# Performance work log

Hardware: AMD Instinct MI355X
Metric: run time of the kernel (lower is better)

## Reference

```python
import jax, jax.numpy as jnp
import numpy as np

P_BU = 0.5  # y_bottom_up_percent
P_TD = 1.0 - P_BU
EPS = 1e-12


def l2n(w):
    # F.normalize(w, dim=1)
    n = jnp.linalg.norm(w, axis=1, keepdims=True)
    return w / jnp.maximum(n, EPS)


def setup_inputs() -> dict:
    key = jax.random.key(0)
    ks = jax.random.split(key, 5)
    X, Y, Z = 64 * 64, 16384, 100
    return {
        "x": jax.random.normal(ks[0], (1, 64, 64), dtype=jnp.float32),
        "z": jax.random.randint(ks[1], (1,), 0, Z, dtype=jnp.int64 if jax.config.jax_enable_x64 else jnp.int32).astype(jnp.int32),
        "per_item": 10,
        "x2y_w": jax.random.uniform(ks[2], (Y, X), dtype=jnp.float32),
        "z2y_w": jax.random.uniform(ks[3], (Y, Z), dtype=jnp.float32),
        "y2z_w": jax.random.uniform(ks[4], (Z, Y), dtype=jnp.float32),
        "age_y": jnp.zeros((Y,), dtype=jnp.float32),
        "age_z": jnp.zeros((Z,), dtype=jnp.float32),
        "thr": jnp.zeros((Y,), dtype=jnp.float32),
    }


def _train_loop(xv, zh, z_idx, per_item, x2y_w, z2y_w, y2z_w, age_y, age_z, thr):
    Y = age_y.shape[0]

    def step(carry, _):
        x2y_w, z2y_w, y2z_w, age_y, age_z, thr = carry
        x2y_w = l2n(x2y_w)
        z2y_w = l2n(z2y_w)
        y2z_w = l2n(y2z_w)
        # pre-response: bottom-up + top-down, shape [Y]
        y_pre = (P_BU * (xv @ x2y_w.T) + P_TD * (zh @ z2y_w.T))[0]
        i0 = jnp.argmax(y_pre)
        r0 = y_pre[i0]
        # top_k_competition(flag=1): keep winner if above threshold or young
        keep = (r0 > thr[i0]) | (age_y[i0] < 1.0)
        unact = jnp.where(age_y >= 1.0, 0.0, 1.0)
        has_unact = jnp.sum(unact) > 0
        alt = jnp.argmax(y_pre * unact)
        win = jnp.where(keep, i0, jnp.where(has_unact, alt, i0))
        # Hebbian/EMA row updates with lr = 1/(age+1) (age before increment)
        lr = 1.0 / (age_y[win] + 1.0)
        x2y_w = x2y_w.at[win].set((1.0 - lr) * x2y_w[win] + lr * xv[0])
        z2y_w = z2y_w.at[win].set((1.0 - lr) * z2y_w[win] + lr * zh[0])
        age_y = age_y.at[win].add(1.0)
        zlr = (1.0 / (age_z[z_idx] + 1.0)) * zh[0, z_idx]
        y_onehot = jnp.zeros((Y,), x2y_w.dtype).at[win].set(1.0)
        y2z_w = y2z_w.at[z_idx].set((1.0 - zlr) * y2z_w[z_idx] + zlr * y_onehot)
        age_z = age_z.at[z_idx].add(1.0)
        thr = thr.at[win].set(lr * r0 + (1.0 - lr) * thr[win])
        return (x2y_w, z2y_w, y2z_w, age_y, age_z, thr), None

    carry, _ = jax.lax.scan(step, (x2y_w, z2y_w, y2z_w, age_y, age_z, thr), None, length=per_item)
    return carry


def reference(x, z, per_item, x2y_w, z2y_w, y2z_w, age_y, age_z, thr):
    # mode == 'train' path of DN.forward, batch = 1
    xv = x.reshape(1, -1)
    xv = xv / jnp.maximum(jnp.linalg.norm(xv, axis=1, keepdims=True), EPS)
    Z = z2y_w.shape[1]
    zh = jax.nn.one_hot(z, Z, dtype=xv.dtype)  # one-hot is already unit L2 norm
    z_idx = z[0]

    x2y_w, z2y_w, y2z_w, age_y, age_z, thr = _train_loop(
        xv, zh, z_idx, per_item, x2y_w, z2y_w, y2z_w, age_y, age_z, thr)

    x2y_w = l2n(x2y_w)
    y2z_w = l2n(y2z_w)
    y_flag = jnp.where(age_y >= 1.0, 1.0, 0.0)  # activated-neuron mask
    y_temp = (xv @ x2y_w.T) * y_flag[None, :]
    # top_k_competition(flag=0): one-hot at argmax
    y = jnp.zeros_like(y_temp).at[0, jnp.argmax(y_temp[0])].set(1.0)
    output = y @ y2z_w.T  # trans_y forward is identity on y_act
    y_activated_num = jnp.sum(y_flag)
    return output, y_activated_num
```

## Files before the change

kernel.cpp:

```cpp
#include <hip/hip_runtime.h>
#include <cmath>

#define EPSN 1e-12f
#define CHUNK 128
#define NCH 128
#define NTL 128
#define MAPCAP 32

__device__ __forceinline__ void amax_combine(float& v, int& i, float ov, int oi) {
    if (ov > v || (ov == v && oi < i)) { v = ov; i = oi; }
}
__device__ __forceinline__ void wave_amax(float& v, int& i) {
    for (int off = 32; off; off >>= 1) {
        float a = __shfl_down(v, off, 64);
        int b = __shfl_down(i, off, 64);
        amax_combine(v, i, a, b);
    }
}

__global__ __launch_bounds__(256) void k_prep(
    const float* __restrict__ x2y, const float* __restrict__ z2y,
    const float* __restrict__ y2z, const int* __restrict__ zptr,
    const float* __restrict__ x,
    float* __restrict__ dotx, float* __restrict__ nw2,
    float* __restrict__ valz, float* __restrict__ nz2,
    float* __restrict__ nry, float* __restrict__ xn2, int* __restrict__ cnti,
    int X, int Y, int Z)
{
    const int bid = blockIdx.x;
    const int NBZ = Y / 4;
    const int tid = threadIdx.x;
    const int lane = tid & 63, wv = tid >> 6;
    if (bid < NBZ) {
        const int zv = zptr[0];
        const int row = bid * 4 + wv;
        const float* r = z2y + (size_t)row * Z;
        float q = 0.f, v = 0.f;
        for (int j = lane; j < Z; j += 64) {
            float e = r[j];
            q += e * e;
            if (j == zv) v = e;
        }
        for (int off = 32; off; off >>= 1) {
            q += __shfl_down(q, off, 64);
            v += __shfl_down(v, off, 64);
        }
        if (lane == 0) { nz2[row] = q; valz[row] = v; }
    } else if (bid < NBZ + Z) {
        const int row = bid - NBZ;
        const float4* r4 = (const float4*)(y2z + (size_t)row * Y);
        float q = 0.f;
        for (int i = tid; i < (Y >> 2); i += 256) {
            float4 w = r4[i];
            q += w.x*w.x + w.y*w.y + w.z*w.z + w.w*w.w;
        }
        for (int off = 32; off; off >>= 1) q += __shfl_down(q, off, 64);
        __shared__ float sq[4];
        if (lane == 0) sq[wv] = q;
        __syncthreads();
        if (tid == 0) nry[row] = sq[0] + sq[1] + sq[2] + sq[3];
    } else if (bid < NBZ + Z + Y) {
        const int row = bid - NBZ - Z;
        const float4* w4 = (const float4*)(x2y + (size_t)row * X);
        const float4* x4 = (const float4*)x;
        float d = 0.f, q = 0.f;
        for (int i = tid; i < (X >> 2); i += 256) {
            float4 w = w4[i]; float4 xx = x4[i];
            d += w.x*xx.x + w.y*xx.y + w.z*xx.z + w.w*xx.w;
            q += w.x*w.x + w.y*w.y + w.z*w.z + w.w*w.w;
        }
        for (int off = 32; off; off >>= 1) {
            d += __shfl_down(d, off, 64);
            q += __shfl_down(q, off, 64);
        }
        __shared__ float sd[4], sq2[4];
        if (lane == 0) { sd[wv] = d; sq2[wv] = q; }
        __syncthreads();
        if (tid == 0) {
            dotx[row] = sd[0] + sd[1] + sd[2] + sd[3];
            nw2[row]  = sq2[0] + sq2[1] + sq2[2] + sq2[3];
        }
    } else {
        const float4* x4 = (const float4*)x;
        float q = 0.f;
        for (int i = tid; i < (X >> 2); i += 256) {
            float4 xx = x4[i];
            q += xx.x*xx.x + xx.y*xx.y + xx.z*xx.z + xx.w*xx.w;
        }
        for (int off = 32; off; off >>= 1) q += __shfl_down(q, off, 64);
        __shared__ float sq3[4];
        if (lane == 0) sq3[wv] = q;
        __syncthreads();
        if (tid == 0) { xn2[0] = sq3[0]+sq3[1]+sq3[2]+sq3[3]; cnti[0] = 0; }
    }
}

__global__ __launch_bounds__(NTL) void k_combine(
    const float* __restrict__ age_y_in,
    const float* __restrict__ dotx, const float* __restrict__ nw2,
    const float* __restrict__ valz, const float* __restrict__ nz2,
    const float* __restrict__ xn2,
    float* __restrict__ yp_ws, float* __restrict__ cA_ws,
    float* __restrict__ chv, int* __restrict__ chi,
    float* __restrict__ chcv, int* __restrict__ chci,
    int* __restrict__ cnti)
{
    const int b = blockIdx.x, t = threadIdx.x;
    const int e = b * CHUNK + t;
    const int lane = t & 63, wv = t >> 6;
    const float xn = fmaxf(sqrtf(xn2[0]), EPSN);
    const float c = dotx[e] / (fmaxf(sqrtf(nw2[e]), EPSN) * xn);
    const float s = valz[e] / fmaxf(sqrtf(nz2[e]), EPSN);
    const float ypv = 0.5f * (c + s);
    const float agev = age_y_in[e];
    const int young = agev < 1.0f;
    cA_ws[e] = c;
    yp_ws[e] = ypv;
    float v1 = ypv; int i1 = e;
    float v2 = c * (young ? 0.0f : 1.0f); int i2 = e;
    int yc = young;
    wave_amax(v1, i1);
    wave_amax(v2, i2);
    for (int off = 32; off; off >>= 1) yc += __shfl_down(yc, off, 64);
    __shared__ float s1v[2]; __shared__ int s1i[2];
    __shared__ float s2v[2]; __shared__ int s2i[2];
    __shared__ int syc[2];
    if (lane == 0) { s1v[wv] = v1; s1i[wv] = i1; s2v[wv] = v2; s2i[wv] = i2; syc[wv] = yc; }
    __syncthreads();
    if (t == 0) {
        float a = s1v[0]; int ai = s1i[0];
        amax_combine(a, ai, s1v[1], s1i[1]);
        float bmv = s2v[0]; int bmi = s2i[0];
        amax_combine(bmv, bmi, s2v[1], s2i[1]);
        chv[b] = a; chi[b] = ai; chcv[b] = bmv; chci[b] = bmi;
        atomicAdd(cnti, syc[0] + syc[1]);
    }
}

#define UPD(WIN, Gthr, Gage, Gvz, Gnz, Gy2z, Gc) do { \
    const int w_ = (WIN); \
    float age_o = (Gage), thr_o = (Gthr), c_o = (Gc); \
    float s_o = (Gvz) / fmaxf(sqrtf((Gnz)), EPSN); \
    int e_ = -1; \
    const int wmn_ = sh_wmn; \
    for (int k_ = 0; k_ < wmn_; ++k_) if (wm_idx[k_] == w_) { \
        age_o = wm_age[k_]; thr_o = wm_thr[k_]; s_o = wm_s[k_]; c_o = wm_c[k_]; e_ = k_; break; } \
    const float lr_ = 1.f/(age_o+1.f), om_ = 1.f-lr_; \
    const float cn_ = (om_*c_o+lr_)/fmaxf(sqrtf(om_*om_+lr_*lr_+2.f*lr_*om_*c_o), EPSN); \
    const float sn_ = (om_*s_o+lr_)/fmaxf(sqrtf(om_*om_+lr_*lr_+2.f*lr_*om_*s_o), EPSN); \
    if (e_ < 0) { e_ = wmn_; wm_idx[e_] = w_; sh_wmn = wmn_ + 1; } \
    wm_age[e_] = age_o + 1.f; wm_thr[e_] = lr_*r0 + om_*thr_o; \
    wm_s[e_] = sn_; wm_c[e_] = cn_; wm_yp[e_] = 0.5f*(cn_+sn_); \
    if (age_o < 1.f && age_o + 1.f >= 1.f) cnt--; \
    { const int cw_ = w_ >> 7; \
      float vv_ = chcv_l[cw_]; int ii_ = chci_l[cw_]; \
      amax_combine(vv_, ii_, cn_, w_); \
      chcv_l[cw_] = vv_; chci_l[cw_] = ii_; } \
    const float L_ = fmaxf(sqrtf(beta*beta*N0sq + 2.f*beta*Aacc + Bacc), EPSN); \
    beta /= L_; Aacc /= L_; Bacc /= (L_*L_); \
    for (int k_ = 0; k_ < ym_n; ++k_) ym_g[k_] /= L_; \
    const float zlr_ = 1.f/(agez+1.f), oz_ = 1.f-zlr_; \
    beta *= oz_; Aacc *= oz_; Bacc *= oz_*oz_; \
    for (int k_ = 0; k_ < ym_n; ++k_) ym_g[k_] *= oz_; \
    int q_ = 0; for (; q_ < ym_n; ++q_) if (ym_idx[q_] == w_) break; \
    if (q_ == ym_n) { ym_idx[q_] = w_; ym_g[q_] = 0.f; ym_v0[q_] = (Gy2z); ym_n++; } \
    const float gold_ = ym_g[q_]; \
    Bacc += 2.f*zlr_*gold_ + zlr_*zlr_; \
    Aacc += zlr_*ym_v0[q_]; \
    ym_g[q_] = gold_ + zlr_; \
    agez += 1.f; \
    sh_win = w_; \
} while (0)

__global__ __launch_bounds__(NTL) void k_loop(
    const int* __restrict__ zptr, const int* __restrict__ pitem,
    const float* __restrict__ y2z,
    const float* __restrict__ age_y_in, const float* __restrict__ age_z_in,
    const float* __restrict__ thr_in,
    const float* __restrict__ valz, const float* __restrict__ nz2,
    const float* __restrict__ nry,
    const float* __restrict__ yp_ws, const float* __restrict__ cA_ws,
    const float* __restrict__ chv, const int* __restrict__ chi,
    const float* __restrict__ chcv, const int* __restrict__ chci,
    const int* __restrict__ cnti,
    float* __restrict__ out, int Y, int Z)
{
    __shared__ float chv_l[NCH]; __shared__ int chi_l[NCH];
    __shared__ float chcv_l[NCH]; __shared__ int chci_l[NCH];
    __shared__ float pthr[NCH], page[NCH], pvz[NCH], pnz[NCH], pyz[NCH], pca[NCH];
    __shared__ float rv[2]; __shared__ int ri[2];
    __shared__ int   wm_idx[MAPCAP];
    __shared__ float wm_age[MAPCAP], wm_thr[MAPCAP], wm_s[MAPCAP], wm_c[MAPCAP], wm_yp[MAPCAP];
    __shared__ int   ym_idx[MAPCAP];
    __shared__ float ym_g[MAPCAP], ym_v0[MAPCAP];
    __shared__ float sh_outz, sh_actn;
    __shared__ int sh_win, sh_winf, sh_flag, sh_wmn;

    const int tid = threadIdx.x, lane = tid & 63, wv = tid >> 6;
    const int zv = zptr[0];
    const float* __restrict__ y2zrow = y2z + (size_t)zv * Y;

    chv_l[tid]  = chv[tid];  chi_l[tid]  = chi[tid];
    chcv_l[tid] = chcv[tid]; chci_l[tid] = chci[tid];
    if (tid == 0) sh_wmn = 0;
    __syncthreads();

    int cnt = 0, ym_n = 0;
    float beta = 1.f, Aacc = 0.f, Bacc = 0.f, N0sq = 0.f, agez = 0.f;
    float r0 = 0.f; int i0 = 0;
    if (tid == 0) { cnt = cnti[0]; N0sq = nry[zv]; agez = age_z_in[zv]; }

    const int PI = pitem[0];
    for (int t = 0; t < PI; ++t) {
        const int ci = chi_l[tid];
        pthr[tid] = thr_in[ci];  page[tid] = age_y_in[ci];
        pvz[tid]  = valz[ci];    pnz[tid]  = nz2[ci];
        pyz[tid]  = y2zrow[ci];  pca[tid]  = cA_ws[ci];
        float v = chv_l[tid]; int i = chi_l[tid];
        wave_amax(v, i);
        if (lane == 0) { rv[wv] = v; ri[wv] = i; }
        __syncthreads();
        if (tid == 0) {
            r0 = rv[0]; i0 = ri[0];
            amax_combine(r0, i0, rv[1], ri[1]);
            const int ts = i0 >> 7;
            float age0 = page[ts], thr0 = pthr[ts];
            for (int k = 0; k < sh_wmn; ++k)
                if (wm_idx[k] == i0) { age0 = wm_age[k]; thr0 = wm_thr[k]; break; }
            const bool keep = (r0 > thr0) || (age0 < 1.f);
            if (keep) {
                UPD(i0, pthr[ts], page[ts], pvz[ts], pnz[ts], pyz[ts], pca[ts]);
                sh_flag = 0;
            } else sh_flag = 1;
        }
        __syncthreads();
        if (sh_flag) {
            float mv = -INFINITY; int mi = 0;
            const int wmn = sh_wmn;
            for (int j = 0; j < Y / NTL; ++j) {
                const int e = j * NTL + tid;
                float vv = yp_ws[e];
                float ag = age_y_in[e];
                for (int k = 0; k < wmn; ++k)
                    if (wm_idx[k] == e) { vv = wm_yp[k]; ag = wm_age[k]; break; }
                const float m = vv * (ag < 1.f ? 1.f : 0.f);
                if (m > mv) { mv = m; mi = e; }
            }
            wave_amax(mv, mi);
            if (lane == 0) { rv[wv] = mv; ri[wv] = mi; }
            __syncthreads();
            if (tid == 0) {
                float av = rv[0]; int alt = ri[0];
                amax_combine(av, alt, rv[1], ri[1]);
                if (cnt > 0) {
                    const float gthr = thr_in[alt], gage = age_y_in[alt];
                    const float gvz = valz[alt],  gnz = nz2[alt];
                    const float gy  = y2zrow[alt], gc = cA_ws[alt];
                    UPD(alt, gthr, gage, gvz, gnz, gy, gc);
                } else {
                    const int ts = i0 >> 7;
                    UPD(i0, pthr[ts], page[ts], pvz[ts], pnz[ts], pyz[ts], pca[ts]);
                }
            }
            __syncthreads();
        }
        const int cw = sh_win >> 7;
        {
            const int e = cw * CHUNK + tid;
            float vv = yp_ws[e];
            const int wmn = sh_wmn;
            for (int k = 0; k < wmn; ++k) if (wm_idx[k] == e) { vv = wm_yp[k]; break; }
            int ii = e;
            wave_amax(vv, ii);
            if (lane == 0) { rv[wv] = vv; ri[wv] = ii; }
        }
        __syncthreads();
        if (tid == 0) {
            float vv = rv[0]; int ii = ri[0];
            amax_combine(vv, ii, rv[1], ri[1]);
            chv_l[cw] = vv; chi_l[cw] = ii;
        }
        __syncthreads();
    }

    {
        float v = chcv_l[tid]; int i = chci_l[tid];
        wave_amax(v, i);
        if (lane == 0) { rv[wv] = v; ri[wv] = i; }
    }
    __syncthreads();
    if (tid == 0) {
        float v = rv[0]; int i = ri[0];
        amax_combine(v, i, rv[1], ri[1]);
        sh_winf = i;
        sh_actn = (float)Y - (float)cnt;
        const float L = fmaxf(sqrtf(beta*beta*N0sq + 2.f*beta*Aacc + Bacc), EPSN);
        float g = 0.f, v0wf = 0.f; bool found = false;
        for (int k = 0; k < ym_n; ++k)
            if (ym_idx[k] == i) { g = ym_g[k]; v0wf = ym_v0[k]; found = true; break; }
        if (!found) v0wf = y2zrow[i];
        sh_outz = (beta * v0wf + g) / L;
    }
    __syncthreads();
    if (tid < Z) {
        float o = (tid == zv) ? sh_outz
                : y2z[(size_t)tid * (size_t)Y + sh_winf] / fmaxf(sqrtf(nry[tid]), EPSN);
        out[tid] = o;
    }
    if (tid == 0) out[Z] = sh_actn;
}

extern "C" void kernel_launch(void* const* d_in, const int* in_sizes, int n_in,
                              void* d_out, int out_size, void* d_ws, size_t ws_size,
                              hipStream_t stream) {
    const float* x    = (const float*)d_in[0];
    const int*   z    = (const int*)d_in[1];
    const int*   pit  = (const int*)d_in[2];
    const float* x2y  = (const float*)d_in[3];
    const float* z2y  = (const float*)d_in[4];
    const float* y2z  = (const float*)d_in[5];
    const float* agey = (const float*)d_in[6];
    const float* agez = (const float*)d_in[7];
    const float* thr  = (const float*)d_in[8];
    const int X = in_sizes[0];
    const int Y = in_sizes[6];
    const int Z = in_sizes[7];

    float* ws = (float*)d_ws;
    float* dotx = ws;
    float* nw2  = ws + (size_t)Y;
    float* valz = ws + 2*(size_t)Y;
    float* nz2  = ws + 3*(size_t)Y;
    float* nry  = ws + 4*(size_t)Y;
    float* xn2  = ws + 4*(size_t)Y + 128;
    int*   cnti = (int*)(ws + 4*(size_t)Y + 129);
    float* ypw  = ws + 4*(size_t)Y + 256;
    float* cAw  = ws + 5*(size_t)Y + 256;
    float* chv  = ws + 6*(size_t)Y + 256;
    int*   chi  = (int*)(ws + 6*(size_t)Y + 384);
    float* chcv = ws + 6*(size_t)Y + 512;
    int*   chci = (int*)(ws + 6*(size_t)Y + 640);
    float* out  = (float*)d_out;

    const int NBZ = Y / 4;
    const int grid_prep = NBZ + Z + Y + 1;
    hipLaunchKernelGGL(k_prep, dim3(grid_prep), dim3(256), 0, stream,
                       x2y, z2y, y2z, z, x, dotx, nw2, valz, nz2, nry, xn2, cnti, X, Y, Z);
    hipLaunchKernelGGL(k_combine, dim3(Y / CHUNK), dim3(NTL), 0, stream,
                       agey, dotx, nw2, valz, nz2, xn2, ypw, cAw, chv, chi, chcv, chci, cnti);
    hipLaunchKernelGGL(k_loop, dim3(1), dim3(NTL), 0, stream,
                       z, pit, y2z, agey, agez, thr, valz, nz2, nry,
                       ypw, cAw, chv, chi, chcv, chci, cnti, out, Y, Z);
}
```

Measured before the change: 88.46 us.

## Run sequential loop as a single wavefront with register-resident maps

The serial per-item loop kernel now runs as one 64-lane wavefront. Shared-memory arrays and __syncthreads barriers are replaced by per-lane registers, shuffles and fully unrolled fixed-size register maps, with map capacity cut from 32 to 16. The combine kernel also gathers the per-chunk winner's threshold, age, z-values and y2z entry, so the loop no longer re-gathers them every iteration. This targets barrier and LDS latency on the serial critical path, at the cost of more register pressure and a smaller map capacity that could overflow if per_item grows.

```diff
diff --git a/kernel.cpp b/kernel.cpp
--- a/kernel.cpp
+++ b/kernel.cpp
@@ -5,7 +5,7 @@
 #define CHUNK 128
 #define NCH 128
 #define NTL 128
-#define MAPCAP 32
+#define MAPCAP 16
 
 __device__ __forceinline__ void amax_combine(float& v, int& i, float ov, int oi) {
     if (ov > v || (ov == v && oi < i)) { v = ov; i = oi; }
@@ -96,21 +96,29 @@
 }
 
 __global__ __launch_bounds__(NTL) void k_combine(
-    const float* __restrict__ age_y_in,
+    const float* __restrict__ age_y_in, const float* __restrict__ thr_in,
+    const float* __restrict__ y2z, const int* __restrict__ zptr,
     const float* __restrict__ dotx, const float* __restrict__ nw2,
     const float* __restrict__ valz, const float* __restrict__ nz2,
     const float* __restrict__ xn2,
     float* __restrict__ yp_ws, float* __restrict__ cA_ws,
     float* __restrict__ chv, int* __restrict__ chi,
     float* __restrict__ chcv, int* __restrict__ chci,
-    int* __restrict__ cnti)
+    float* __restrict__ cthr, float* __restrict__ cage,
+    float* __restrict__ cvz, float* __restrict__ cnz,
+    float* __restrict__ cyz, float* __restrict__ ccc,
+    int* __restrict__ cnti, int Y)
 {
     const int b = blockIdx.x, t = threadIdx.x;
     const int e = b * CHUNK + t;
     const int lane = t & 63, wv = t >> 6;
+    const int zv = zptr[0];
     const float xn = fmaxf(sqrtf(xn2[0]), EPSN);
+    const float vz_e = valz[e], nz_e = nz2[e];
+    const float thr_e = thr_in[e];
+    const float yz_e = y2z[(size_t)zv * Y + e];
     const float c = dotx[e] / (fmaxf(sqrtf(nw2[e]), EPSN) * xn);
-    const float s = valz[e] / fmaxf(sqrtf(nz2[e]), EPSN);
+    const float s = vz_e / fmaxf(sqrtf(nz_e), EPSN);
     const float ypv = 0.5f * (c + s);
     const float agev = age_y_in[e];
     const int young = agev < 1.0f;
@@ -124,7 +132,7 @@
     for (int off = 32; off; off >>= 1) yc += __shfl_down(yc, off, 64);
     __shared__ float s1v[2]; __shared__ int s1i[2];
     __shared__ float s2v[2]; __shared__ int s2i[2];
-    __shared__ int syc[2];
+    __shared__ int syc[2]; __shared__ int sh_c1;
     if (lane == 0) { s1v[wv] = v1; s1i[wv] = i1; s2v[wv] = v2; s2i[wv] = i2; syc[wv] = yc; }
     __syncthreads();
     if (t == 0) {
@@ -133,7 +141,13 @@
         float bmv = s2v[0]; int bmi = s2i[0];
         amax_combine(bmv, bmi, s2v[1], s2i[1]);
         chv[b] = a; chi[b] = ai; chcv[b] = bmv; chci[b] = bmi;
+        sh_c1 = ai;
         atomicAdd(cnti, syc[0] + syc[1]);
+    }
+    __syncthreads();
+    if (e == sh_c1) {
+        cthr[b] = thr_e; cage[b] = agev; cvz[b] = vz_e;
+        cnz[b] = nz_e;   cyz[b] = yz_e;  ccc[b] = c;
     }
 }
 
@@ -142,37 +156,49 @@
     float age_o = (Gage), thr_o = (Gthr), c_o = (Gc); \
     float s_o = (Gvz) / fmaxf(sqrtf((Gnz)), EPSN); \
     int e_ = -1; \
-    const int wmn_ = sh_wmn; \
-    for (int k_ = 0; k_ < wmn_; ++k_) if (wm_idx[k_] == w_) { \
-        age_o = wm_age[k_]; thr_o = wm_thr[k_]; s_o = wm_s[k_]; c_o = wm_c[k_]; e_ = k_; break; } \
+    _Pragma("unroll") \
+    for (int k_ = 0; k_ < MAPCAP; ++k_) if (wmI[k_] == w_) { \
+        age_o = wmAge[k_]; thr_o = wmThr[k_]; s_o = wmS[k_]; c_o = wmC[k_]; e_ = k_; } \
     const float lr_ = 1.f/(age_o+1.f), om_ = 1.f-lr_; \
     const float cn_ = (om_*c_o+lr_)/fmaxf(sqrtf(om_*om_+lr_*lr_+2.f*lr_*om_*c_o), EPSN); \
     const float sn_ = (om_*s_o+lr_)/fmaxf(sqrtf(om_*om_+lr_*lr_+2.f*lr_*om_*s_o), EPSN); \
-    if (e_ < 0) { e_ = wmn_; wm_idx[e_] = w_; sh_wmn = wmn_ + 1; } \
-    wm_age[e_] = age_o + 1.f; wm_thr[e_] = lr_*r0 + om_*thr_o; \
-    wm_s[e_] = sn_; wm_c[e_] = cn_; wm_yp[e_] = 0.5f*(cn_+sn_); \
+    if (e_ < 0) { e_ = wmn; wmn++; } \
+    _Pragma("unroll") \
+    for (int k_ = 0; k_ < MAPCAP; ++k_) if (k_ == e_) { \
+        wmI[k_] = w_; wmAge[k_] = age_o + 1.f; wmThr[k_] = lr_*r0 + om_*thr_o; \
+        wmS[k_] = sn_; wmC[k_] = cn_; wmYp[k_] = 0.5f*(cn_+sn_); } \
     if (age_o < 1.f && age_o + 1.f >= 1.f) cnt--; \
-    { const int cw_ = w_ >> 7; \
-      float vv_ = chcv_l[cw_]; int ii_ = chci_l[cw_]; \
-      amax_combine(vv_, ii_, cn_, w_); \
-      chcv_l[cw_] = vv_; chci_l[cw_] = ii_; } \
+    { const int cw_ = (w_) >> 7; \
+      if (lane == (cw_ & 63)) { \
+        if (cw_ & 64) amax_combine(chc1, chcI1, cn_, w_); \
+        else          amax_combine(chc0, chcI0, cn_, w_); } } \
     const float L_ = fmaxf(sqrtf(beta*beta*N0sq + 2.f*beta*Aacc + Bacc), EPSN); \
     beta /= L_; Aacc /= L_; Bacc /= (L_*L_); \
-    for (int k_ = 0; k_ < ym_n; ++k_) ym_g[k_] /= L_; \
+    _Pragma("unroll") \
+    for (int k_ = 0; k_ < MAPCAP; ++k_) ymG[k_] /= L_; \
     const float zlr_ = 1.f/(agez+1.f), oz_ = 1.f-zlr_; \
     beta *= oz_; Aacc *= oz_; Bacc *= oz_*oz_; \
-    for (int k_ = 0; k_ < ym_n; ++k_) ym_g[k_] *= oz_; \
-    int q_ = 0; for (; q_ < ym_n; ++q_) if (ym_idx[q_] == w_) break; \
-    if (q_ == ym_n) { ym_idx[q_] = w_; ym_g[q_] = 0.f; ym_v0[q_] = (Gy2z); ym_n++; } \
-    const float gold_ = ym_g[q_]; \
+    _Pragma("unroll") \
+    for (int k_ = 0; k_ < MAPCAP; ++k_) ymG[k_] *= oz_; \
+    int q_ = -1; \
+    _Pragma("unroll") \
+    for (int k_ = 0; k_ < MAPCAP; ++k_) if (ymI[k_] == w_) q_ = k_; \
+    if (q_ < 0) { q_ = ymn; ymn++; \
+        _Pragma("unroll") \
+        for (int k_ = 0; k_ < MAPCAP; ++k_) if (k_ == q_) { \
+            ymI[k_] = w_; ymG[k_] = 0.f; ymV0[k_] = (Gy2z); } } \
+    float gold_ = 0.f, v0_ = 0.f; \
+    _Pragma("unroll") \
+    for (int k_ = 0; k_ < MAPCAP; ++k_) if (k_ == q_) { gold_ = ymG[k_]; v0_ = ymV0[k_]; } \
     Bacc += 2.f*zlr_*gold_ + zlr_*zlr_; \
-    Aacc += zlr_*ym_v0[q_]; \
-    ym_g[q_] = gold_ + zlr_; \
+    Aacc += zlr_*v0_; \
+    _Pragma("unroll") \
+    for (int k_ = 0; k_ < MAPCAP; ++k_) if (k_ == q_) ymG[k_] = gold_ + zlr_; \
     agez += 1.f; \
-    sh_win = w_; \
+    win = w_; \
 } while (0)
 
-__global__ __launch_bounds__(NTL) void k_loop(
+__global__ __launch_bounds__(64) void k_loop(
     const int* __restrict__ zptr, const int* __restrict__ pitem,
     const float* __restrict__ y2z,
     const float* __restrict__ age_y_in, const float* __restrict__ age_z_in,
@@ -180,134 +206,132 @@
     const float* __restrict__ valz, const float* __restrict__ nz2,
     const float* __restrict__ nry,
     const float* __restrict__ yp_ws, const float* __restrict__ cA_ws,
-    const float* __restrict__ chv, const int* __restrict__ chi,
-    const float* __restrict__ chcv, const int* __restrict__ chci,
+    const float* __restrict__ chv_g, const int* __restrict__ chi_g,
+    const float* __restrict__ chcv_g, const int* __restrict__ chci_g,
+    const float* __restrict__ cthr, const float* __restrict__ cage,
+    const float* __restrict__ cvz, const float* __restrict__ cnz,
+    const float* __restrict__ cyz, const float* __restrict__ ccc,
     const int* __restrict__ cnti,
     float* __restrict__ out, int Y, int Z)
 {
-    __shared__ float chv_l[NCH]; __shared__ int chi_l[NCH];
-    __shared__ float chcv_l[NCH]; __shared__ int chci_l[NCH];
-    __shared__ float pthr[NCH], page[NCH], pvz[NCH], pnz[NCH], pyz[NCH], pca[NCH];
-    __shared__ float rv[2]; __shared__ int ri[2];
-    __shared__ int   wm_idx[MAPCAP];
-    __shared__ float wm_age[MAPCAP], wm_thr[MAPCAP], wm_s[MAPCAP], wm_c[MAPCAP], wm_yp[MAPCAP];
-    __shared__ int   ym_idx[MAPCAP];
-    __shared__ float ym_g[MAPCAP], ym_v0[MAPCAP];
-    __shared__ float sh_outz, sh_actn;
-    __shared__ int sh_win, sh_winf, sh_flag, sh_wmn;
-
-    const int tid = threadIdx.x, lane = tid & 63, wv = tid >> 6;
+    const int lane = threadIdx.x;
     const int zv = zptr[0];
     const float* __restrict__ y2zrow = y2z + (size_t)zv * Y;
 
-    chv_l[tid]  = chv[tid];  chi_l[tid]  = chi[tid];
-    chcv_l[tid] = chcv[tid]; chci_l[tid] = chci[tid];
-    if (tid == 0) sh_wmn = 0;
-    __syncthreads();
-
-    int cnt = 0, ym_n = 0;
-    float beta = 1.f, Aacc = 0.f, Bacc = 0.f, N0sq = 0.f, agez = 0.f;
-    float r0 = 0.f; int i0 = 0;
-    if (tid == 0) { cnt = cnti[0]; N0sq = nry[zv]; agez = age_z_in[zv]; }
+    float chv0 = chv_g[lane], chv1 = chv_g[lane + 64];
+    int   chi0 = chi_g[lane], chi1 = chi_g[lane + 64];
+    float chc0 = chcv_g[lane], chc1 = chcv_g[lane + 64];
+    int   chcI0 = chci_g[lane], chcI1 = chci_g[lane + 64];
+    float pthr0 = cthr[lane], pthr1 = cthr[lane + 64];
+    float page0 = cage[lane], page1 = cage[lane + 64];
+    float pvz0  = cvz[lane],  pvz1  = cvz[lane + 64];
+    float pnz0  = cnz[lane],  pnz1  = cnz[lane + 64];
+    float pyz0  = cyz[lane],  pyz1  = cyz[lane + 64];
+    float pca0  = ccc[lane],  pca1  = ccc[lane + 64];
+
+    int cnt = cnti[0];
+    float N0sq = nry[zv], agez = age_z_in[zv];
+    float beta = 1.f, Aacc = 0.f, Bacc = 0.f;
+    int wmn = 0, ymn = 0;
+    int   wmI[MAPCAP]; float wmAge[MAPCAP], wmThr[MAPCAP], wmS[MAPCAP], wmC[MAPCAP], wmYp[MAPCAP];
+    int   ymI[MAPCAP]; float ymG[MAPCAP], ymV0[MAPCAP];
+#pragma unroll
+    for (int k = 0; k < MAPCAP; ++k) {
+        wmI[k] = -1; wmAge[k] = 0.f; wmThr[k] = 0.f; wmS[k] = 0.f; wmC[k] = 0.f; wmYp[k] = 0.f;
+        ymI[k] = -1; ymG[k] = 0.f; ymV0[k] = 0.f;
+    }
 
     const int PI = pitem[0];
     for (int t = 0; t < PI; ++t) {
-        const int ci = chi_l[tid];
-        pthr[tid] = thr_in[ci];  page[tid] = age_y_in[ci];
-        pvz[tid]  = valz[ci];    pnz[tid]  = nz2[ci];
-        pyz[tid]  = y2zrow[ci];  pca[tid]  = cA_ws[ci];
-        float v = chv_l[tid]; int i = chi_l[tid];
+        float v = chv0; int i = chi0;
+        amax_combine(v, i, chv1, chi1);
         wave_amax(v, i);
-        if (lane == 0) { rv[wv] = v; ri[wv] = i; }
-        __syncthreads();
-        if (tid == 0) {
-            r0 = rv[0]; i0 = ri[0];
-            amax_combine(r0, i0, rv[1], ri[1]);
-            const int ts = i0 >> 7;
-            float age0 = page[ts], thr0 = pthr[ts];
-            for (int k = 0; k < sh_wmn; ++k)
-                if (wm_idx[k] == i0) { age0 = wm_age[k]; thr0 = wm_thr[k]; break; }
-            const bool keep = (r0 > thr0) || (age0 < 1.f);
-            if (keep) {
-                UPD(i0, pthr[ts], page[ts], pvz[ts], pnz[ts], pyz[ts], pca[ts]);
-                sh_flag = 0;
-            } else sh_flag = 1;
-        }
-        __syncthreads();
-        if (sh_flag) {
+        const float r0 = __shfl(v, 0);
+        const int   i0 = __shfl(i, 0);
+        const int ts = i0 >> 7;
+        const int sl = ts & 63;
+        const bool hi = (ts & 64) != 0;
+        const float bthr = __shfl(hi ? pthr1 : pthr0, sl);
+        const float bage = __shfl(hi ? page1 : page0, sl);
+        const float bvz  = __shfl(hi ? pvz1  : pvz0,  sl);
+        const float bnz  = __shfl(hi ? pnz1  : pnz0,  sl);
+        const float byz  = __shfl(hi ? pyz1  : pyz0,  sl);
+        const float bca  = __shfl(hi ? pca1  : pca0,  sl);
+        float age0 = bage, thr0 = bthr;
+#pragma unroll
+        for (int k = 0; k < MAPCAP; ++k)
+            if (wmI[k] == i0) { age0 = wmAge[k]; thr0 = wmThr[k]; }
+        const bool keep = (r0 > thr0) || (age0 < 1.f);
+        int win;
+        if (keep) {
+            UPD(i0, bthr, bage, bvz, bnz, byz, bca);
+        } else {
             float mv = -INFINITY; int mi = 0;
-            const int wmn = sh_wmn;
-            for (int j = 0; j < Y / NTL; ++j) {
-                const int e = j * NTL + tid;
+            for (int e = lane; e < Y; e += 64) {
                 float vv = yp_ws[e];
                 float ag = age_y_in[e];
-                for (int k = 0; k < wmn; ++k)
-                    if (wm_idx[k] == e) { vv = wm_yp[k]; ag = wm_age[k]; break; }
+#pragma unroll
+                for (int k = 0; k < MAPCAP; ++k)
+                    if (wmI[k] == e) { vv = wmYp[k]; ag = wmAge[k]; }
                 const float m = vv * (ag < 1.f ? 1.f : 0.f);
-                if (m > mv) { mv = m; mi = e; }
+                amax_combine(mv, mi, m, e);
             }
             wave_amax(mv, mi);
-            if (lane == 0) { rv[wv] = mv; ri[wv] = mi; }
-            __syncthreads();
-            if (tid == 0) {
-                float av = rv[0]; int alt = ri[0];
-                amax_combine(av, alt, rv[1], ri[1]);
-                if (cnt > 0) {
-                    const float gthr = thr_in[alt], gage = age_y_in[alt];
-                    const float gvz = valz[alt],  gnz = nz2[alt];
-                    const float gy  = y2zrow[alt], gc = cA_ws[alt];
-                    UPD(alt, gthr, gage, gvz, gnz, gy, gc);
-                } else {
-                    const int ts = i0 >> 7;
-                    UPD(i0, pthr[ts], page[ts], pvz[ts], pnz[ts], pyz[ts], pca[ts]);
-                }
+            const int alt = __shfl(mi, 0);
+            if (cnt > 0) {
+                const float gthr = thr_in[alt], gage = age_y_in[alt];
+                const float gvz = valz[alt],   gnz = nz2[alt];
+                const float gy  = y2zrow[alt], gc = cA_ws[alt];
+                UPD(alt, gthr, gage, gvz, gnz, gy, gc);
+            } else {
+                UPD(i0, bthr, bage, bvz, bnz, byz, bca);
             }
-            __syncthreads();
-        }
-        const int cw = sh_win >> 7;
-        {
-            const int e = cw * CHUNK + tid;
-            float vv = yp_ws[e];
-            const int wmn = sh_wmn;
-            for (int k = 0; k < wmn; ++k) if (wm_idx[k] == e) { vv = wm_yp[k]; break; }
-            int ii = e;
-            wave_amax(vv, ii);
-            if (lane == 0) { rv[wv] = vv; ri[wv] = ii; }
-        }
-        __syncthreads();
-        if (tid == 0) {
-            float vv = rv[0]; int ii = ri[0];
-            amax_combine(vv, ii, rv[1], ri[1]);
-            chv_l[cw] = vv; chi_l[cw] = ii;
-        }
-        __syncthreads();
-    }
-
-    {
-        float v = chcv_l[tid]; int i = chci_l[tid];
-        wave_amax(v, i);
-        if (lane == 0) { rv[wv] = v; ri[wv] = i; }
-    }
-    __syncthreads();
-    if (tid == 0) {
-        float v = rv[0]; int i = ri[0];
-        amax_combine(v, i, rv[1], ri[1]);
-        sh_winf = i;
-        sh_actn = (float)Y - (float)cnt;
-        const float L = fmaxf(sqrtf(beta*beta*N0sq + 2.f*beta*Aacc + Bacc), EPSN);
-        float g = 0.f, v0wf = 0.f; bool found = false;
-        for (int k = 0; k < ym_n; ++k)
-            if (ym_idx[k] == i) { g = ym_g[k]; v0wf = ym_v0[k]; found = true; break; }
-        if (!found) v0wf = y2zrow[i];
-        sh_outz = (beta * v0wf + g) / L;
-    }
-    __syncthreads();
-    if (tid < Z) {
-        float o = (tid == zv) ? sh_outz
-                : y2z[(size_t)tid * (size_t)Y + sh_winf] / fmaxf(sqrtf(nry[tid]), EPSN);
-        out[tid] = o;
-    }
-    if (tid == 0) out[Z] = sh_actn;
+        }
+        const int cw = win >> 7;
+        const int base = cw * CHUNK;
+        float vA = yp_ws[base + lane];
+        float vB = yp_ws[base + 64 + lane];
+        int iA = base + lane, iB = base + 64 + lane;
+#pragma unroll
+        for (int k = 0; k < MAPCAP; ++k) {
+            if (wmI[k] == iA) vA = wmYp[k];
+            if (wmI[k] == iB) vB = wmYp[k];
+        }
+        amax_combine(vA, iA, vB, iB);
+        wave_amax(vA, iA);
+        const float nv = __shfl(vA, 0);
+        const int   ni = __shfl(iA, 0);
+        const float nthr = thr_in[ni], nage = age_y_in[ni];
+        const float nvz = valz[ni],   nnz = nz2[ni];
+        const float nyz = y2zrow[ni], nca = cA_ws[ni];
+        if (lane == (cw & 63)) {
+            if (cw & 64) {
+                chv1 = nv; chi1 = ni;
+                pthr1 = nthr; page1 = nage; pvz1 = nvz; pnz1 = nnz; pyz1 = nyz; pca1 = nca;
+            } else {
+                chv0 = nv; chi0 = ni;
+                pthr0 = nthr; page0 = nage; pvz0 = nvz; pnz0 = nnz; pyz0 = nyz; pca0 = nca;
+            }
+        }
+    }
+
+    float fv = chc0; int fi = chcI0;
+    amax_combine(fv, fi, chc1, chcI1);
+    wave_amax(fv, fi);
+    const int winf = __shfl(fi, 0);
+    const float actn = (float)Y - (float)cnt;
+    const float L = fmaxf(sqrtf(beta*beta*N0sq + 2.f*beta*Aacc + Bacc), EPSN);
+    float g = 0.f, v0wf = y2zrow[winf];
+#pragma unroll
+    for (int k = 0; k < MAPCAP; ++k)
+        if (ymI[k] == winf) { g = ymG[k]; v0wf = ymV0[k]; }
+    const float outz = (beta * v0wf + g) / L;
+    for (int e = lane; e < Z; e += 64) {
+        const float o = (e == zv) ? outz
+            : y2z[(size_t)e * Y + winf] / fmaxf(sqrtf(nry[e]), EPSN);
+        out[e] = o;
+    }
+    if (lane == 0) out[Z] = actn;
 }
 
 extern "C" void kernel_launch(void* const* d_in, const int* in_sizes, int n_in,
@@ -336,10 +360,17 @@
     int*   cnti = (int*)(ws + 4*(size_t)Y + 129);
     float* ypw  = ws + 4*(size_t)Y + 256;
     float* cAw  = ws + 5*(size_t)Y + 256;
-    float* chv  = ws + 6*(size_t)Y + 256;
-    int*   chi  = (int*)(ws + 6*(size_t)Y + 384);
-    float* chcv = ws + 6*(size_t)Y + 512;
-    int*   chci = (int*)(ws + 6*(size_t)Y + 640);
+    float* base6 = ws + 6*(size_t)Y + 256;
+    float* chv  = base6;
+    int*   chi  = (int*)(base6 + NCH);
+    float* chcv = base6 + 2*NCH;
+    int*   chci = (int*)(base6 + 3*NCH);
+    float* cthr = base6 + 4*NCH;
+    float* cage = base6 + 5*NCH;
+    float* cvz  = base6 + 6*NCH;
+    float* cnz  = base6 + 7*NCH;
+    float* cyz  = base6 + 8*NCH;
+    float* ccc  = base6 + 9*NCH;
     float* out  = (float*)d_out;
 
     const int NBZ = Y / 4;
@@ -347,8 +378,11 @@
     hipLaunchKernelGGL(k_prep, dim3(grid_prep), dim3(256), 0, stream,
                        x2y, z2y, y2z, z, x, dotx, nw2, valz, nz2, nry, xn2, cnti, X, Y, Z);
     hipLaunchKernelGGL(k_combine, dim3(Y / CHUNK), dim3(NTL), 0, stream,
-                       agey, dotx, nw2, valz, nz2, xn2, ypw, cAw, chv, chi, chcv, chci, cnti);
-    hipLaunchKernelGGL(k_loop, dim3(1), dim3(NTL), 0, stream,
+                       agey, thr, y2z, z, dotx, nw2, valz, nz2, xn2,
+                       ypw, cAw, chv, chi, chcv, chci,
+                       cthr, cage, cvz, cnz, cyz, ccc, cnti, Y);
+    hipLaunchKernelGGL(k_loop, dim3(1), dim3(64), 0, stream,
                        z, pit, y2z, agey, agez, thr, valz, nz2, nry,
-                       ypw, cAw, chv, chi, chcv, chci, cnti, out, Y, Z);
-}
+                       ypw, cAw, chv, chi, chcv, chci,
+                       cthr, cage, cvz, cnz, cyz, ccc, cnti, out, Y, Z);
+}
```

Result: no change. 88.34 us (-0.1%).
